# Kernel tuning notes

Measured on AMD Instinct MI355X. Metric: run time of the kernel, lower is better.

The kernel has to match this reference:

```python
import jax, jax.numpy as jnp
import numpy as np

TEMPERATURE = 34.0
B, CREF, CIN, COUT, KK, KSZ, H, W = 16, 256, 256, 256, 4, 3, 56, 56
HIDDEN = int(CIN * 0.25) + 1  # 65, since ref_in_planes != 3


def setup_inputs() -> dict:
    key = jax.random.key(0)
    ks = jax.random.split(key, 7)
    ref = jax.random.normal(ks[0], (B, CREF, H, W), dtype=jnp.float32)
    x = jax.random.normal(ks[1], (B, CIN, H, W), dtype=jnp.float32)
    fc1_w = jax.random.normal(ks[2], (HIDDEN, CREF), dtype=jnp.float32) * (2.0 / CREF) ** 0.5
    fc2_w = jax.random.normal(ks[3], (KK, HIDDEN), dtype=jnp.float32) * (2.0 / HIDDEN) ** 0.5
    fc2_b = jnp.zeros((KK,), dtype=jnp.float32)
    weight = jax.random.normal(ks[4], (KK, COUT, CIN, KSZ, KSZ), dtype=jnp.float32) * 0.02
    bias = jnp.zeros((KK, COUT), dtype=jnp.float32)
    return {"ref": ref, "x": x, "fc1_w": fc1_w, "fc2_w": fc2_w,
            "fc2_b": fc2_b, "weight": weight, "bias": bias}


def _attention(ref, fc1_w, fc2_w, fc2_b):
    pooled = jnp.mean(ref, axis=(2, 3))                 # [B, CREF] adaptive avgpool to 1x1
    h = jax.nn.relu(pooled @ fc1_w.T)                   # [B, HIDDEN] (1x1 conv == matmul)
    logits = h @ fc2_w.T + fc2_b                        # [B, K]
    return jax.nn.softmax(logits / TEMPERATURE, axis=-1)


def _conv_one(xi, wi):
    # xi: [CIN, H, W], wi: [COUT, CIN, k, k]; stride 1, padding 1, dilation 1, groups 1
    out = jax.lax.conv_general_dilated(
        xi[None], wi, window_strides=(1, 1), padding=((1, 1), (1, 1)),
        dimension_numbers=("NCHW", "OIHW", "NCHW"))
    return out[0]


def reference(ref, x, fc1_w, fc2_w, fc2_b, weight, bias):
    attn = _attention(ref, fc1_w, fc2_w, fc2_b)                  # [B, K]
    agg_w = jnp.einsum("bk,koihw->boihw", attn, weight)          # per-sample kernels
    agg_b = attn @ bias                                          # [B, COUT]
    out = jax.vmap(_conv_one)(x, agg_w)                          # [B, COUT, H, W]
    return out + agg_b[:, :, None, None]
```

## Files before the change

kernel.cpp:

```cpp
#include <hip/hip_runtime.h>
#include <hip/hip_bf16.h>

#define BB    16
#define CREF  256
#define CINC  256
#define COUTC 256
#define KKN   4
#define HH    56
#define WWW   56
#define HIDDEN 65
#define NPIX  3136
#define PPIX  3364
#define TEMP  34.0f

typedef __bf16 bf16x8 __attribute__((ext_vector_type(8)));
typedef float  f32x4  __attribute__((ext_vector_type(4)));

#define WS_ATTN   0
#define WS_AGGB   4096
#define WS_POOL   24576
#define WS_AGGW   65536
#define WS_XPAD   19005440

#define ABUF  73728
#define XB_SZ 24576
#define ASLOT 8192
#define LDS_TOT (2*XB_SZ + 4*ASLOT)

__global__ void pool_k(const float* __restrict__ ref, float* __restrict__ pooled,
                       __bf16* __restrict__ xpad) {
    int wid = threadIdx.x >> 6, lane = threadIdx.x & 63;
    int gw = blockIdx.x * 4 + wid;
    const float4* r4 = reinterpret_cast<const float4*>(ref) + (size_t)gw * 784;
    float s = 0.f;
    for (int i = lane; i < 784; i += 64) {
        float4 v = r4[i];
        s += v.x + v.y + v.z + v.w;
    }
    for (int o = 32; o; o >>= 1) s += __shfl_xor(s, o);
    if (lane == 0) pooled[gw] = s * (1.0f / (float)NPIX);

    if (gw < 3648) {
        int b = gw / 228, i = gw % 228;
        int ph, pw;
        if (i < 58)       { ph = 0;        pw = i; }
        else if (i < 116) { ph = 57;       pw = i - 58; }
        else if (i < 172) { ph = i - 115;  pw = 0; }
        else              { ph = i - 171;  pw = 57; }
        uint2* dst = (uint2*)(xpad + ((size_t)b * PPIX + ph * 58 + pw) * 256);
        dst[lane] = (uint2){0u, 0u};
    }
}

__global__ void attn_k(const float* __restrict__ pooled, const float* __restrict__ fc1w,
                       const float* __restrict__ fc2w, const float* __restrict__ fc2b,
                       const float* __restrict__ bias,
                       float* __restrict__ attn, float* __restrict__ aggb) {
    int b = blockIdx.x;
    int t = threadIdx.x;
    __shared__ float sh[HIDDEN + 7];
    __shared__ float sl[KKN];
    __shared__ float sa[KKN];
    const float* prow = pooled + b * CREF;
    {
        int j = t >> 2, sub = t & 3;
        const float4* w4 = (const float4*)(fc1w + j * CREF + sub * 64);
        const float4* p4 = (const float4*)(prow + sub * 64);
        float s = 0.f;
#pragma unroll
        for (int k = 0; k < 16; ++k) {
            float4 w = w4[k], p = p4[k];
            s += w.x * p.x + w.y * p.y + w.z * p.z + w.w * p.w;
        }
        s += __shfl_xor(s, 1); s += __shfl_xor(s, 2);
        if (sub == 0) sh[j] = fmaxf(s, 0.f);
    }
    if (t < 4) {
        const float4* w4 = (const float4*)(fc1w + 64 * CREF + t * 64);
        const float4* p4 = (const float4*)(prow + t * 64);
        float s = 0.f;
#pragma unroll
        for (int k = 0; k < 16; ++k) {
            float4 w = w4[k], p = p4[k];
            s += w.x * p.x + w.y * p.y + w.z * p.z + w.w * p.w;
        }
        s += __shfl_xor(s, 1); s += __shfl_xor(s, 2);
        if (t == 0) sh[64] = fmaxf(s, 0.f);
    }
    __syncthreads();
    if (t < KKN) {
        float s = fc2b[t];
        for (int j = 0; j < HIDDEN; ++j) s += sh[j] * fc2w[t * HIDDEN + j];
        sl[t] = s * (1.0f / TEMP);
    }
    __syncthreads();
    if (t == 0) {
        float m = fmaxf(fmaxf(sl[0], sl[1]), fmaxf(sl[2], sl[3]));
        float e0 = expf(sl[0] - m), e1 = expf(sl[1] - m);
        float e2 = expf(sl[2] - m), e3 = expf(sl[3] - m);
        float inv = 1.f / (e0 + e1 + e2 + e3);
        sa[0] = e0 * inv; sa[1] = e1 * inv; sa[2] = e2 * inv; sa[3] = e3 * inv;
        attn[b * 4 + 0] = sa[0]; attn[b * 4 + 1] = sa[1];
        attn[b * 4 + 2] = sa[2]; attn[b * 4 + 3] = sa[3];
    }
    __syncthreads();
    {
        float s = 0.f;
#pragma unroll
        for (int k = 0; k < KKN; ++k) s += sa[k] * bias[k * COUTC + t];
        aggb[b * COUTC + t] = s;
    }
}

__global__ void aggw_k(const float* __restrict__ attn, const float* __restrict__ weight,
                       __bf16* __restrict__ aggw) {
    __shared__ float s_attn[64];
    int t = threadIdx.x;
    int co = t >> 5, cr = t & 31;
    int cout = blockIdx.x * 8 + co;
    int cb8 = blockIdx.y;
    int cin = cb8 * 32 + cr;
    if (t < 64) s_attn[t] = attn[t];
    __syncthreads();
    float w[4][9];
#pragma unroll
    for (int k = 0; k < 4; ++k) {
        const float* wp = weight + ((size_t)(k * 256 + cout) * 256 + cin) * 9;
#pragma unroll
        for (int tp = 0; tp < 9; ++tp) w[k][tp] = wp[tp];
    }
    int ch = cout >> 7, coutl = cout & 127;
    int cing = cr >> 3, cinr = cr & 7;
    for (int b = 0; b < BB; ++b) {
        float a0 = s_attn[b * 4 + 0], a1 = s_attn[b * 4 + 1];
        float a2 = s_attn[b * 4 + 2], a3 = s_attn[b * 4 + 3];
#pragma unroll
        for (int tap = 0; tap < 9; ++tap) {
            float v = a0 * w[0][tap] + a1 * w[1][tap] + a2 * w[2][tap] + a3 * w[3][tap];
            size_t e = (size_t)((b * 2 + ch) * 8 + cb8) * 36864 +
                       (tap * 4 + cing) * 1024 + coutl * 8 + cinr;
            aggw[e] = (__bf16)v;
        }
    }
}

__global__ void xpad_int_k(const float* __restrict__ x, __bf16* __restrict__ xpad) {
    __shared__ float tile[64][65];
    int pt = blockIdx.x;
    int cg = blockIdx.y;
    int b  = blockIdx.z;
    int q = threadIdx.x >> 6, l = threadIdx.x & 63;
    for (int k = 0; k < 16; ++k) {
        int cl = q * 16 + k;
        tile[cl][l] = x[((size_t)(b * 256 + cg * 64 + cl)) * NPIX + pt * 64 + l];
    }
    __syncthreads();
    for (int k = 0; k < 16; ++k) {
        int pl = q * 16 + k;
        int pixel = pt * 64 + pl;
        int h = pixel / 56, w = pixel - h * 56;
        xpad[(((size_t)b * PPIX + (h + 1) * 58 + (w + 1)) * 256) + cg * 64 + l] =
            (__bf16)tile[l][pl];
    }
}

__global__ __launch_bounds__(256, 2) void conv_k(const __bf16* __restrict__ xpad,
                                                 const __bf16* __restrict__ aggw,
                                                 const float* __restrict__ aggb,
                                                 float* __restrict__ out) {
    extern __shared__ __attribute__((aligned(16))) char smem[];
    char* xs = smem;
    char* as = smem + 2 * XB_SZ;

    const int orig = blockIdx.x;
    const int logical = (orig & 7) * 56 + (orig >> 3);
    const int b  = logical / 28;
    const int r  = logical - b * 28;
    const int rp = r >> 1;
    const int ch = r & 1;
    const int tid = threadIdx.x;
    const int wid = tid >> 6, lane = tid & 63;
    const int l15 = lane & 15, l4 = lane >> 4;
    const int h0 = rp * 4;

    const char* xb  = (const char*)xpad + (size_t)b * PPIX * 512;
    const char* awb = (const char*)aggw + (size_t)((b * 2 + ch) * 8) * ABUF;

    f32x4 acc[8][4];
#pragma unroll
    for (int m = 0; m < 8; ++m)
#pragma unroll
        for (int n = 0; n < 4; ++n) acc[m][n] = (f32x4){0.f, 0.f, 0.f, 0.f};

    bf16x8 af[2][8];
    bf16x8 bfr[2][4];

    auto XSTAGE = [&](int buf, int c) {
#pragma unroll
        for (int j = 0; j < 6; ++j) {
            const char* src = xb + (size_t)((h0 + j) * 58 + lane) * 512 + c * 64 + wid * 16;
            __builtin_amdgcn_global_load_lds(
                (const __attribute__((address_space(1))) void*)src,
                (__attribute__((address_space(3))) void*)(xs + buf * XB_SZ + (wid * 6 + j) * 1024),
                16, 0, 0);
        }
    };
    auto ASTAGE = [&](int slot, int c, int tap) {
#pragma unroll
        for (int j = 0; j < 2; ++j) {
            int k = wid * 2 + j;
            const char* src = awb + (size_t)c * ABUF + tap * 8192 + k * 1024 + lane * 16;
            __builtin_amdgcn_global_load_lds(
                (const __attribute__((address_space(1))) void*)src,
                (__attribute__((address_space(3))) void*)(as + slot * ASLOT + k * 1024),
                16, 0, 0);
        }
    };

#define ALOADF(P, SLOT) do { \
    const char* ap_ = as + (SLOT) * ASLOT + l4 * 2048 + l15 * 16; \
    _Pragma("unroll") \
    for (int m_ = 0; m_ < 8; ++m_) af[P][m_] = *(const bf16x8*)(ap_ + m_ * 256); \
} while (0)

#define BLOADF(P, T, LB) do { \
    const int kh_ = (T) / 3, kw_ = (T) - kh_ * 3; \
    _Pragma("unroll") \
    for (int nf_ = 0; nf_ < 4; ++nf_) \
        bfr[P][nf_] = *(const bf16x8*)((LB) + \
            (((l4 * 6 + wid + kh_) * 64) + nf_ * 16 + l15 + kw_) * 16); \
} while (0)

#define MFMAS(P) do { \
    __builtin_amdgcn_s_setprio(1); \
    _Pragma("unroll") \
    for (int nf_ = 0; nf_ < 4; ++nf_) \
        _Pragma("unroll") \
        for (int m_ = 0; m_ < 8; ++m_) \
            acc[m_][nf_] = __builtin_amdgcn_mfma_f32_16x16x32_bf16( \
                af[P][m_], bfr[P][nf_], acc[m_][nf_], 0, 0, 0); \
    __builtin_amdgcn_s_setprio(0); \
} while (0)

#define SUBBAR(N) do { \
        asm volatile("s_waitcnt vmcnt(" #N ")" ::: "memory"); \
        __builtin_amdgcn_s_barrier(); \
        __builtin_amdgcn_sched_barrier(0); } while (0)

    XSTAGE(0, 0);
    ASTAGE(0, 0, 0);
    ASTAGE(1, 0, 1);
    ASTAGE(2, 0, 2);
    SUBBAR(0);
    ALOADF(0, 0);
    BLOADF(0, 0, xs);

    int cur = 0;
    for (int c = 0; c < 8; ++c) {
        const int cs = c & 3;
        const char* lb  = xs + cur * XB_SZ;
        const char* lbn = xs + (cur ^ 1) * XB_SZ;
#pragma unroll
        for (int t = 0; t < 9; ++t) {
            const int p = t & 1, q = p ^ 1;
            if (t < 6) {
                ASTAGE((t + cs + 3) & 3, c, t + 3);
            } else if (c < 7) {
                ASTAGE((t + cs + 3) & 3, c + 1, t - 6);
            }
            if (t == 5 && c < 7) XSTAGE(cur ^ 1, c + 1);
            if (t < 8) {
                ALOADF(q, (t + 1 + cs) & 3);
                BLOADF(q, t + 1, lb);
            } else if (c < 7) {
                ALOADF(q, (cs + 1) & 3);
                BLOADF(q, 0, lbn);
            }
            MFMAS(p);
            if (t <= 4)      { SUBBAR(2); }
            else if (t == 5) { if (c < 7) SUBBAR(8); else SUBBAR(2); }
            else if (t == 6) { if (c < 7) SUBBAR(8); else SUBBAR(0); }
            else if (t == 7) { if (c < 7) SUBBAR(2); else SUBBAR(0); }
            else             { if (c < 7) SUBBAR(2);  }
        }
        if (c < 7) {
#pragma unroll
            for (int m = 0; m < 8; ++m) af[0][m] = af[1][m];
#pragma unroll
            for (int n = 0; n < 4; ++n) bfr[0][n] = bfr[1][n];
        }
        cur ^= 1;
    }
#undef ALOADF
#undef BLOADF
#undef MFMAS
#undef SUBBAR

    const int row = rp * 4 + wid;
#pragma unroll
    for (int m = 0; m < 8; ++m) {
#pragma unroll
        for (int i = 0; i < 4; ++i) {
            int cout = ch * 128 + m * 16 + l4 * 4 + i;
            float bv = aggb[b * COUTC + cout];
            float* op = out + ((size_t)(b * COUTC + cout) * NPIX + row * 56);
#pragma unroll
            for (int nf = 0; nf < 3; ++nf)
                __builtin_nontemporal_store(acc[m][nf][i] + bv, op + nf * 16 + l15);
            if (l15 < 8)
                __builtin_nontemporal_store(acc[m][3][i] + bv, op + 48 + l15);
        }
    }
}

extern "C" void kernel_launch(void* const* d_in, const int* in_sizes, int n_in,
                              void* d_out, int out_size, void* d_ws, size_t ws_size,
                              hipStream_t stream) {
    (void)in_sizes; (void)n_in; (void)out_size; (void)ws_size;
    const float* ref    = (const float*)d_in[0];
    const float* x      = (const float*)d_in[1];
    const float* fc1w   = (const float*)d_in[2];
    const float* fc2w   = (const float*)d_in[3];
    const float* fc2b   = (const float*)d_in[4];
    const float* weight = (const float*)d_in[5];
    const float* bias   = (const float*)d_in[6];
    float* out = (float*)d_out;
    char* ws = (char*)d_ws;

    float*  attn   = (float*)(ws + WS_ATTN);
    float*  aggb   = (float*)(ws + WS_AGGB);
    float*  pooled = (float*)(ws + WS_POOL);
    __bf16* aggw   = (__bf16*)(ws + WS_AGGW);
    __bf16* xpad   = (__bf16*)(ws + WS_XPAD);

    hipFuncSetAttribute((const void*)conv_k,
                        hipFuncAttributeMaxDynamicSharedMemorySize, LDS_TOT);

    pool_k<<<1024, 256, 0, stream>>>(ref, pooled, xpad);
    attn_k<<<16, 256, 0, stream>>>(pooled, fc1w, fc2w, fc2b, bias, attn, aggb);
    aggw_k<<<dim3(32, 8), 256, 0, stream>>>(attn, weight, aggw);
    xpad_int_k<<<dim3(49, 4, 16), 256, 0, stream>>>(x, xpad);
    conv_k<<<448, 256, LDS_TOT, stream>>>(xpad, aggw, aggb, out);
}
```

Measured before the change: 103.0 us.

## Drop register double-buffering of MFMA fragments and restructure barrier schedule

Replaces the two-stage register prefetch of A and B fragments with single-buffered loads issued right before each MFMA block, followed by an explicit lgkmcnt wait. The global-to-LDS staging and vmcnt barriers are reordered so barriers come before the fragment loads. This roughly halves fragment register usage and removes the copy between buffers at each channel chunk, which could help occupancy or reduce spills. In exchange, LDS read latency is no longer hidden behind the previous tap's MFMAs.

```diff
diff --git a/kernel.cpp b/kernel.cpp
--- a/kernel.cpp
+++ b/kernel.cpp
@@ -192,8 +192,8 @@
 #pragma unroll
         for (int n = 0; n < 4; ++n) acc[m][n] = (f32x4){0.f, 0.f, 0.f, 0.f};
 
-    bf16x8 af[2][8];
-    bf16x8 bfr[2][4];
+    bf16x8 af[8];
+    bf16x8 bfr[4];
 
     auto XSTAGE = [&](int buf, int c) {
 #pragma unroll
@@ -217,34 +217,38 @@
         }
     };
 
-#define ALOADF(P, SLOT) do { \
+#define ALOADF(SLOT) do { \
     const char* ap_ = as + (SLOT) * ASLOT + l4 * 2048 + l15 * 16; \
     _Pragma("unroll") \
-    for (int m_ = 0; m_ < 8; ++m_) af[P][m_] = *(const bf16x8*)(ap_ + m_ * 256); \
+    for (int m_ = 0; m_ < 8; ++m_) af[m_] = *(const bf16x8*)(ap_ + m_ * 256); \
 } while (0)
 
-#define BLOADF(P, T, LB) do { \
+#define BLOADF(T, LB) do { \
     const int kh_ = (T) / 3, kw_ = (T) - kh_ * 3; \
     _Pragma("unroll") \
     for (int nf_ = 0; nf_ < 4; ++nf_) \
-        bfr[P][nf_] = *(const bf16x8*)((LB) + \
+        bfr[nf_] = *(const bf16x8*)((LB) + \
             (((l4 * 6 + wid + kh_) * 64) + nf_ * 16 + l15 + kw_) * 16); \
 } while (0)
 
-#define MFMAS(P) do { \
+#define MFMAS() do { \
     __builtin_amdgcn_s_setprio(1); \
     _Pragma("unroll") \
     for (int nf_ = 0; nf_ < 4; ++nf_) \
         _Pragma("unroll") \
         for (int m_ = 0; m_ < 8; ++m_) \
             acc[m_][nf_] = __builtin_amdgcn_mfma_f32_16x16x32_bf16( \
-                af[P][m_], bfr[P][nf_], acc[m_][nf_], 0, 0, 0); \
+                af[m_], bfr[nf_], acc[m_][nf_], 0, 0, 0); \
     __builtin_amdgcn_s_setprio(0); \
 } while (0)
 
 #define SUBBAR(N) do { \
         asm volatile("s_waitcnt vmcnt(" #N ")" ::: "memory"); \
         __builtin_amdgcn_s_barrier(); \
+        __builtin_amdgcn_sched_barrier(0); } while (0)
+
+#define LGKM0 do { \
+        asm volatile("s_waitcnt lgkmcnt(0)" ::: "memory"); \
         __builtin_amdgcn_sched_barrier(0); } while (0)
 
     XSTAGE(0, 0);
@@ -252,42 +256,31 @@
     ASTAGE(1, 0, 1);
     ASTAGE(2, 0, 2);
     SUBBAR(0);
-    ALOADF(0, 0);
-    BLOADF(0, 0, xs);
 
     int cur = 0;
     for (int c = 0; c < 8; ++c) {
         const int cs = c & 3;
-        const char* lb  = xs + cur * XB_SZ;
-        const char* lbn = xs + (cur ^ 1) * XB_SZ;
+        const char* lb = xs + cur * XB_SZ;
 #pragma unroll
         for (int t = 0; t < 9; ++t) {
-            const int p = t & 1, q = p ^ 1;
-            if (t < 6) {
-                ASTAGE((t + cs + 3) & 3, c, t + 3);
-            } else if (c < 7) {
-                ASTAGE((t + cs + 3) & 3, c + 1, t - 6);
+            if (c < 7) {
+                if (t < 6) ASTAGE((t + cs + 3) & 3, c, t + 3);
+                else       ASTAGE((t + cs + 3) & 3, c + 1, t - 6);
+                if (t == 5) XSTAGE(cur ^ 1, c + 1);
+            } else {
+                if (t < 6) ASTAGE((t + cs + 3) & 3, 7, t + 3);
             }
-            if (t == 5 && c < 7) XSTAGE(cur ^ 1, c + 1);
-            if (t < 8) {
-                ALOADF(q, (t + 1 + cs) & 3);
-                BLOADF(q, t + 1, lb);
-            } else if (c < 7) {
-                ALOADF(q, (cs + 1) & 3);
-                BLOADF(q, 0, lbn);
+            ALOADF((t + cs) & 3);
+            BLOADF(t, lb);
+            if (c < 7) {
+                if (t <= 4 || t == 8) SUBBAR(4); else SUBBAR(10);
+            } else {
+                if (t <= 5)      { SUBBAR(4); }
+                else if (t == 6) { SUBBAR(2); }
+                else if (t == 7) { SUBBAR(0); }
             }
-            MFMAS(p);
-            if (t <= 4)      { SUBBAR(2); }
-            else if (t == 5) { if (c < 7) SUBBAR(8); else SUBBAR(2); }
-            else if (t == 6) { if (c < 7) SUBBAR(8); else SUBBAR(0); }
-            else if (t == 7) { if (c < 7) SUBBAR(2); else SUBBAR(0); }
-            else             { if (c < 7) SUBBAR(2);  }
-        }
-        if (c < 7) {
-#pragma unroll
-            for (int m = 0; m < 8; ++m) af[0][m] = af[1][m];
-#pragma unroll
-            for (int n = 0; n < 4; ++n) bfr[0][n] = bfr[1][n];
+            LGKM0;
+            MFMAS();
         }
         cur ^= 1;
     }
@@ -295,6 +288,7 @@
 #undef BLOADF
 #undef MFMAS
 #undef SUBBAR
+#undef LGKM0
 
     const int row = rp * 4 + wid;
 #pragma unroll
```

Measured after the change: 98.66 us (median of 2 runs). 1.04x faster.
